# Optimization experiments

Measured on AMD Instinct MI355X. Metric: run time of the kernel, lower is better.

The kernel has to match this reference:

```python
import jax, jax.numpy as jnp
import numpy as np
from math import ceil, sqrt

# Inner module: Linear(2048,4096)+ReLU, Linear(4096,4096)+ReLU, Linear(4096,2048)
D_IN, D_H, D_OUT = 2048, 4096, 2048
BATCH = 4096
# named_modules() order: each Linear yields weight then bias; ReLU skipped
SHAPES = [(D_H, D_IN), (D_H,), (D_H, D_H), (D_H,), (D_OUT, D_H), (D_OUT,)]
NUM_P = sum(int(np.prod(s)) for s in SHAPES)  # 33_566_720
SIZE_N = ceil(sqrt(NUM_P))                    # 5794
SIZE_M = ceil(1.0 * SIZE_N / 2)               # 2897 (compress = 1.0)


def setup_inputs() -> dict:
    key = jax.random.key(0)
    k1, k2, k3 = jax.random.split(key, 3)
    k = sqrt(12) / 2 * SIZE_M ** (-0.25)  # norm_V init bound
    V1 = jax.random.uniform(k1, (SIZE_N, SIZE_M), jnp.float32, -k, k)
    V2 = jax.random.uniform(k2, (SIZE_M, SIZE_N), jnp.float32, -k, k)
    x = jax.random.normal(k3, (BATCH, D_IN), jnp.float32)
    return {"x": x, "V1": V1, "V2": V2}


def _unpack(Vf):
    # scatter-copy: contiguous slices of flattened V -> weights/biases in traversal order
    params, i = [], 0
    for s in SHAPES:
        n = int(np.prod(s))
        params.append(Vf[i:i + n].reshape(s))
        i += n
    return params


def reference(x, V1, V2):
    # WandBtoV: low-rank reconstruction then per-element copy into weights (fused here)
    Vf = (V1 @ V2).reshape(-1)  # [SIZE_N*SIZE_N]; only first NUM_P elements used
    W1, b1, W2, b2, W3, b3 = _unpack(Vf)
    h = jax.nn.relu(x @ W1.T + b1)   # [B, D_H]
    h = jax.nn.relu(h @ W2.T + b2)   # [B, D_H]
    return h @ W3.T + b3             # [B, D_OUT]
```

## Files before the change

kernel.cpp:

```cpp
#include <hip/hip_runtime.h>
#include <stdint.h>

typedef __attribute__((ext_vector_type(8)))  __bf16 bf16x8;
typedef __attribute__((ext_vector_type(16))) float  f32x16;
typedef unsigned short u16;
typedef __attribute__((ext_vector_type(8))) unsigned short u16x8;

#define GLOBAL_AS __attribute__((address_space(1)))
#define LDS_AS    __attribute__((address_space(3)))

__device__ __forceinline__ void load_lds16(const void* g, void* l) {
    __builtin_amdgcn_global_load_lds((const GLOBAL_AS void*)g, (LDS_AS void*)l, 16, 0, 0);
}

__device__ __forceinline__ u16 f2bf(float f) {
    union { float f; uint32_t u; } v; v.f = f;
    uint32_t r = v.u + 0x7FFFu + ((v.u >> 16) & 1u);
    return (u16)(r >> 16);
}
__device__ __forceinline__ float b2f(u16 b) {
    union { uint32_t u; float f; } v; v.u = ((uint32_t)b) << 16;
    return v.f;
}

__global__ void k_conv_pad(const float* __restrict__ in, u16* __restrict__ out,
                           int rIn, int cIn, int cOut, int total8) {
    int idx = blockIdx.x * blockDim.x + threadIdx.x;
    if (idx >= total8) return;
    int c8n = cOut >> 3;
    int r  = idx / c8n;
    int c0 = (idx - r * c8n) << 3;
    u16x8 o;
#pragma unroll
    for (int j = 0; j < 8; ++j) {
        int c = c0 + j;
        o[j] = (r < rIn && c < cIn) ? f2bf(in[(size_t)r * cIn + c]) : (u16)0;
    }
    *(u16x8*)(out + (size_t)r * cOut + c0) = o;
}

__global__ void k_transpose_conv(const float* __restrict__ in, u16* __restrict__ out,
                                 int kIn, int nIn, int kOut) {
    __shared__ float tile[32][33];
    int k0 = blockIdx.x * 32, n0 = blockIdx.y * 32;
    int tx = threadIdx.x, ty = threadIdx.y;
#pragma unroll
    for (int i = 0; i < 4; ++i) {
        int k = k0 + ty + i * 8, n = n0 + tx;
        tile[ty + i * 8][tx] = (k < kIn && n < nIn) ? in[(size_t)k * nIn + n] : 0.f;
    }
    __syncthreads();
#pragma unroll
    for (int i = 0; i < 4; ++i) {
        int n = n0 + ty + i * 8, k = k0 + tx;
        out[(size_t)n * kOut + k] = f2bf(tile[tx][ty + i * 8]);
    }
}

template <int MODE>
__global__ __launch_bounds__(256, 4) void k_gemm_bt(
    const u16* __restrict__ A, const u16* __restrict__ B,
    const u16* __restrict__ bias, void* __restrict__ Cv,
    int K, int ldc, int mReal, int nReal) {
    (void)bias;
    __shared__ __align__(16) char lds[32768];
    char* As = lds;
    char* Bs = lds + 16384;

    const int tid  = threadIdx.x;
    const int w    = tid >> 6, lane = tid & 63;
    const int l31  = lane & 31, hi = lane >> 5;
    const int wm   = (w & 1) * 64, wn = (w >> 1) * 64;

    const int id     = blockIdx.y * gridDim.x + blockIdx.x;
    const int gridM  = gridDim.y, gridN = gridDim.x;
    const int GM     = 8;
    const int perSup = GM * gridN;
    const int super  = id / perSup;
    const int rem    = id - super * perSup;
    const int sm0    = super * GM;
    const int smH    = (gridM - sm0 < GM) ? (gridM - sm0) : GM;
    const int tm     = sm0 + rem % smH;
    const int tn     = rem / smH;
    const int bm = tm * 128, bn = tn * 128;

    const int srcRow = tid >> 3;
    const int srcCol = (tid & 7) ^ (srcRow & 7);
    const u16* aSrc = A + (size_t)(bm + srcRow) * K + (srcCol << 3);
    const u16* bSrc = B + (size_t)(bn + srcRow) * K + (srcCol << 3);
    char* aDst = As + ((tid & ~63) << 4);
    char* bDst = Bs + ((tid & ~63) << 4);

    const int aRow0 = (wm + l31) * 128;
    const int aRow1 = (wm + 32 + l31) * 128;
    const int bRow0 = (wn + l31) * 128;
    const int bRow1 = (wn + 32 + l31) * 128;

    f32x16 acc[2][2];
#pragma unroll
    for (int i = 0; i < 2; ++i)
#pragma unroll
        for (int j = 0; j < 2; ++j) acc[i][j] = (f32x16)(0.f);

    for (int k0 = 0; k0 < K; k0 += 64) {
#pragma unroll
        for (int t = 0; t < 4; ++t) {
            load_lds16(aSrc + (size_t)(t * 32) * K, aDst + t * 4096);
            load_lds16(bSrc + (size_t)(t * 32) * K, bDst + t * 4096);
        }
        aSrc += 64; bSrc += 64;
        __syncthreads();
#pragma unroll
        for (int ks = 0; ks < 4; ++ks) {
            const int swz = (((ks * 2 + hi) ^ (l31 & 7)) << 4);
            bf16x8 af[2], bfr[2];
            af[0]  = *(const bf16x8*)(As + aRow0 + swz);
            af[1]  = *(const bf16x8*)(As + aRow1 + swz);
            bfr[0] = *(const bf16x8*)(Bs + bRow0 + swz);
            bfr[1] = *(const bf16x8*)(Bs + bRow1 + swz);
#pragma unroll
            for (int mi = 0; mi < 2; ++mi)
#pragma unroll
                for (int ni = 0; ni < 2; ++ni)
                    acc[mi][ni] = __builtin_amdgcn_mfma_f32_32x32x16_bf16(
                        af[mi], bfr[ni], acc[mi][ni], 0, 0, 0);
        }
        __syncthreads();
    }

    float bv[2];
    if (MODE >= 1) {
#pragma unroll
        for (int ni = 0; ni < 2; ++ni) bv[ni] = b2f(bias[bn + wn + ni * 32 + l31]);
    }
#pragma unroll
    for (int mi = 0; mi < 2; ++mi) {
#pragma unroll
        for (int reg = 0; reg < 16; ++reg) {
            int row = bm + wm + mi * 32 + (reg & 3) + 8 * (reg >> 2) + 4 * hi;
#pragma unroll
            for (int ni = 0; ni < 2; ++ni) {
                int col = bn + wn + ni * 32 + l31;
                float v = acc[mi][ni][reg];
                if (MODE == 0) {
                    if (row < mReal && col < nReal)
                        ((u16*)Cv)[(size_t)row * ldc + col] = f2bf(v);
                } else if (MODE == 1) {
                    v += bv[ni];
                    v = v > 0.f ? v : 0.f;
                    ((u16*)Cv)[(size_t)row * ldc + col] = f2bf(v);
                } else {
                    ((float*)Cv)[(size_t)row * ldc + col] = v + bv[ni];
                }
            }
        }
    }
}

extern "C" void kernel_launch(void* const* d_in, const int* in_sizes, int n_in,
                              void* d_out, int out_size, void* d_ws, size_t ws_size,
                              hipStream_t stream) {
    (void)in_sizes; (void)n_in; (void)out_size; (void)ws_size;
    const float* x  = (const float*)d_in[0];
    const float* V1 = (const float*)d_in[1];
    const float* V2 = (const float*)d_in[2];

    char* ws = (char*)d_ws;
    u16* Vf   = (u16*)(ws);
    u16* V1b  = (u16*)(ws + 67141120);
    u16* V2bT = (u16*)(ws + 67141120 + 34668544);
    u16* Xb   = (u16*)(ws + 67141120 + 2 * 34668544);
    u16* H1   = V1b;
    u16* H2   = V2bT;

    k_conv_pad<<<8464, 256, 0, stream>>>(V1, V1b, 5794, 2897, 2944, 5888 * 2944 / 8);
    k_transpose_conv<<<dim3(92, 184), dim3(32, 8), 0, stream>>>(V2, V2bT, 2897, 5794, 2944);
    k_conv_pad<<<4096, 256, 0, stream>>>(x, Xb, 4096, 2048, 2048, 4096 * 2048 / 8);

    k_gemm_bt<0><<<dim3(46, 46), 256, 0, stream>>>(V1b, V2bT, nullptr, Vf,
                                                   2944, 5794, 5794, 5794);
    k_gemm_bt<1><<<dim3(32, 32), 256, 0, stream>>>(Xb, Vf + 0, Vf + 8388608, H1,
                                                   2048, 4096, 4096, 4096);
    k_gemm_bt<1><<<dim3(32, 32), 256, 0, stream>>>(H1, Vf + 8392704, Vf + 25169920, H2,
                                                   4096, 4096, 4096, 4096);
    k_gemm_bt<2><<<dim3(16, 32), 256, 0, stream>>>(H2, Vf + 25174016, Vf + 33562624, d_out,
                                                   4096, 2048, 4096, 2048);
}
```

Before: 781.8 us.

## Double-buffer LDS tiles in GEMM with two-stage async prefetch

The GEMM kernel now uses a double-buffered 64KB LDS area. It issues global-to-LDS loads two k-steps ahead and waits on vmcnt with explicit s_waitcnt and barriers, so the loads overlap with MFMA work. The aim is to hide global memory latency that the single-buffer load/sync/compute loop left exposed. In exchange, occupancy drops from 4 to 2 blocks per CU, and the code depends on hand-coded waitcnt encodings being correct.

Measured after the change: 798.8 us. 2.2% more time.

```diff
diff --git a/kernel.cpp b/kernel.cpp
--- a/kernel.cpp
+++ b/kernel.cpp
@@ -58,14 +58,12 @@
 }
 
 template <int MODE>
-__global__ __launch_bounds__(256, 4) void k_gemm_bt(
+__global__ __launch_bounds__(256, 2) void k_gemm_bt(
     const u16* __restrict__ A, const u16* __restrict__ B,
     const u16* __restrict__ bias, void* __restrict__ Cv,
     int K, int ldc, int mReal, int nReal) {
     (void)bias;
-    __shared__ __align__(16) char lds[32768];
-    char* As = lds;
-    char* Bs = lds + 16384;
+    __shared__ __align__(16) char lds[65536];
 
     const int tid  = threadIdx.x;
     const int w    = tid >> 6, lane = tid & 63;
@@ -88,8 +86,21 @@
     const int srcCol = (tid & 7) ^ (srcRow & 7);
     const u16* aSrc = A + (size_t)(bm + srcRow) * K + (srcCol << 3);
     const u16* bSrc = B + (size_t)(bn + srcRow) * K + (srcCol << 3);
-    char* aDst = As + ((tid & ~63) << 4);
-    char* bDst = Bs + ((tid & ~63) << 4);
+    const int ldsOff = (tid & ~63) << 4;
+
+    const int nIter = K >> 6;
+
+    auto stage = [&](int j) {
+        char* aD = lds + ((j & 1) << 15) + ldsOff;
+        char* bD = aD + 16384;
+        const u16* aS = aSrc + (j << 6);
+        const u16* bS = bSrc + (j << 6);
+#pragma unroll
+        for (int t = 0; t < 4; ++t) {
+            load_lds16(aS + (size_t)(t * 32) * K, aD + t * 4096);
+            load_lds16(bS + (size_t)(t * 32) * K, bD + t * 4096);
+        }
+    };
 
     const int aRow0 = (wm + l31) * 128;
     const int aRow1 = (wm + 32 + l31) * 128;
@@ -102,22 +113,25 @@
 #pragma unroll
         for (int j = 0; j < 2; ++j) acc[i][j] = (f32x16)(0.f);
 
-    for (int k0 = 0; k0 < K; k0 += 64) {
-#pragma unroll
-        for (int t = 0; t < 4; ++t) {
-            load_lds16(aSrc + (size_t)(t * 32) * K, aDst + t * 4096);
-            load_lds16(bSrc + (size_t)(t * 32) * K, bDst + t * 4096);
-        }
-        aSrc += 64; bSrc += 64;
-        __syncthreads();
+    stage(0);
+    stage(1);
+
+    for (int i = 0; i < nIter; ++i) {
+        if (i < nIter - 1) __builtin_amdgcn_s_waitcnt(0xF78);
+        else               __builtin_amdgcn_s_waitcnt(0xF70);
+        __builtin_amdgcn_s_barrier();
+        __builtin_amdgcn_sched_barrier(0);
+
+        const char* Ac = lds + ((i & 1) << 15);
+        const char* Bc = Ac + 16384;
 #pragma unroll
         for (int ks = 0; ks < 4; ++ks) {
             const int swz = (((ks * 2 + hi) ^ (l31 & 7)) << 4);
             bf16x8 af[2], bfr[2];
-            af[0]  = *(const bf16x8*)(As + aRow0 + swz);
-            af[1]  = *(const bf16x8*)(As + aRow1 + swz);
-            bfr[0] = *(const bf16x8*)(Bs + bRow0 + swz);
-            bfr[1] = *(const bf16x8*)(Bs + bRow1 + swz);
+            af[0]  = *(const bf16x8*)(Ac + aRow0 + swz);
+            af[1]  = *(const bf16x8*)(Ac + aRow1 + swz);
+            bfr[0] = *(const bf16x8*)(Bc + bRow0 + swz);
+            bfr[1] = *(const bf16x8*)(Bc + bRow1 + swz);
 #pragma unroll
             for (int mi = 0; mi < 2; ++mi)
 #pragma unroll
@@ -125,7 +139,10 @@
                     acc[mi][ni] = __builtin_amdgcn_mfma_f32_32x32x16_bf16(
                         af[mi], bfr[ni], acc[mi][ni], 0, 0, 0);
         }
-        __syncthreads();
+
+        __builtin_amdgcn_sched_barrier(0);
+        __builtin_amdgcn_s_barrier();
+        if (i + 2 < nIter) stage(i + 2);
     }
 
     float bv[2];
```
